# Performance work log

Measured on AMD Instinct MI355X. Metric: run time of the kernel, lower is better.

The kernel has to match this reference:

```python
import jax, jax.numpy as jnp
import numpy as np

N = 50000
E = 800000
IN_DIM = 256
HID = 128
HALF = HID // 2
OUT_DIM = 2


def setup_inputs() -> dict:
    key = jax.random.key(0)
    ks = jax.random.split(key, 16)
    s = lambda fan_in: 1.0 / np.sqrt(fan_in)
    inp = {
        "x": jax.random.normal(ks[0], (N, IN_DIM), dtype=jnp.float32),
        "edge_index": jax.random.randint(ks[1], (2, E), 0, N, dtype=jnp.int64),
        # lin_in: input_dim -> hidden
        "W_in": jax.random.uniform(ks[2], (IN_DIM, HID), jnp.float32, -s(IN_DIM), s(IN_DIM)),
        "b_in": jnp.zeros((HID,), jnp.float32),
        # lin_nor / lin_abnor: half -> hidden
        "W_nor": jax.random.uniform(ks[3], (HALF, HID), jnp.float32, -s(HALF), s(HALF)),
        "b_nor": jnp.zeros((HID,), jnp.float32),
        "W_abnor": jax.random.uniform(ks[4], (HALF, HID), jnp.float32, -s(HALF), s(HALF)),
        "b_abnor": jnp.zeros((HID,), jnp.float32),
        # attention gate
        "W_att": jax.random.uniform(ks[5], (HID, HID), jnp.float32, -s(HID), s(HID)),
        "b_att": jnp.zeros((HID,), jnp.float32),
        "v_att": jax.random.uniform(ks[6], (HID, 1), jnp.float32, -s(HID), s(HID)),
        # update linear
        "W_upd": jax.random.uniform(ks[7], (HID, HID), jnp.float32, -s(HID), s(HID)),
        "b_upd": jnp.zeros((HID,), jnp.float32),
        # classifier
        "W_cls": jax.random.uniform(ks[8], (HID, OUT_DIM), jnp.float32, -s(HID), s(HID)),
        "b_cls": jnp.zeros((OUT_DIM,), jnp.float32),
    }
    return inp


def reference(x, edge_index, W_in, b_in, W_nor, b_nor, W_abnor, b_abnor,
              W_att, b_att, v_att, W_upd, b_upd, W_cls, b_cls):
    n = x.shape[0]
    # add self loops (add_self_loops)
    loops = jnp.tile(jnp.arange(n, dtype=edge_index.dtype), (2, 1))
    ei = jnp.concatenate([edge_index, loops], axis=1)
    row, col = ei[0], ei[1]  # row = source j, col = target i

    # lin_in + leaky_relu (dropout p=0 / eval)
    h = jax.nn.leaky_relu(x @ W_in + b_in)

    # split halves and project
    x_nor = h[:, :HALF] @ W_nor + b_nor      # [N, HID]
    x_abnor = h[:, HALF:] @ W_abnor + b_abnor

    # symmetric normalization by target degree
    deg = jax.ops.segment_sum(jnp.ones_like(col, dtype=h.dtype), col, num_segments=n)
    dinv = jnp.where(deg > 0, jax.lax.rsqrt(jnp.where(deg > 0, deg, 1.0)), 0.0)
    norm = dinv[row] * dinv[col]             # [E']

    # per-edge gather
    xn_j = x_nor[row]                        # [E', HID]
    xa_j = x_abnor[row]

    # denoising attention gate: sigmoid(v^T tanh(W(xn+xa)+b))
    h_att = jnp.tanh((xn_j + xa_j) @ W_att + b_att)
    alpha = jax.nn.sigmoid(h_att @ v_att)    # [E', 1]

    msg = norm[:, None] * (alpha * xn_j + (1.0 - alpha) * xa_j)

    # scatter-add to targets
    aggr = jax.ops.segment_sum(msg, col, num_segments=n)  # [N, HID]

    upd = aggr @ W_upd + b_upd
    out = jax.nn.leaky_relu(upd) @ W_cls + b_cls
    return out
```

## Files before the change

### kernel.cpp

```cpp
#include <hip/hip_runtime.h>

#define N_NODES 50000
#define E_EDGES 800000
#define IN_DIM  256
#define HID     128
#define HALF    64
#define OUT_DIM 2
#define NW      32
#define SLOPE   0.01f

#define ST      132
#define WSLICE  (NW * ST)

#define SCAN_B  512
#define SCAN_NB ((N_NODES + SCAN_B - 1) / SCAN_B)

typedef unsigned int uint32;
typedef __attribute__((ext_vector_type(8)))  __bf16 bf16x8v;
typedef __attribute__((ext_vector_type(16))) float  f32x16;

union BF8 { bf16x8v v; unsigned short s[8]; uint4 q; };

#define FI_F 0
#define FN_F 4096
#define FA_F 5120
#define FT_F 6144
#define FU_F 8192
#define F_TOTAL 10240

__device__ __forceinline__ uint32 rne16u(uint32 u) {
    return (u + 0x7fffu + ((u >> 16) & 1u)) >> 16;
}

__device__ __forceinline__ void split8(const float* f, BF8& hi, BF8& lo) {
    #pragma unroll
    for (int j = 0; j < 8; j++) {
        uint32 uu = __float_as_uint(f[j]);
        uint32 h  = rne16u(uu);
        float  fh = __uint_as_float(h << 16);
        float  r  = f[j] - fh;
        hi.s[j] = (unsigned short)h;
        lo.s[j] = (unsigned short)rne16u(__float_as_uint(r));
    }
}

__device__ __forceinline__ void mfma3(f32x16& acc, bf16x8v ah, bf16x8v al,
                                      bf16x8v bh, bf16x8v bl) {
    acc = __builtin_amdgcn_mfma_f32_32x32x16_bf16(ah, bh, acc, 0, 0, 0);
    acc = __builtin_amdgcn_mfma_f32_32x32x16_bf16(ah, bl, acc, 0, 0, 0);
    acc = __builtin_amdgcn_mfma_f32_32x32x16_bf16(al, bh, acc, 0, 0, 0);
}

__device__ __forceinline__ void mfma_gemm(f32x16* acc, const float* B, int aoff,
                                          int S, int sg0, const uint4* __restrict__ F,
                                          int fbase, int l) {
    const int row = l & 31;
    const int khi = 8 * (l >> 5);
    for (int s = 0; s < S; s++) {
        int k0 = aoff + 16 * s + khi;
        float a8[8];
        *(float4*)&a8[0] = *(const float4*)&B[row * ST + k0];
        *(float4*)&a8[4] = *(const float4*)&B[row * ST + k0 + 4];
        BF8 ah, al; split8(a8, ah, al);
        #pragma unroll
        for (int t = 0; t < 4; t++) {
            int f = fbase + ((sg0 + s) * 4 + t) * 64 + l;
            BF8 bh, bl; bh.q = F[2 * f]; bl.q = F[2 * f + 1];
            mfma3(acc[t], ah.v, al.v, bh.v, bl.v);
        }
    }
}

__device__ __forceinline__ void mfma_gemm2(f32x16* acc, const float* B, int aoff,
                                           int S, int sg0, const uint4* __restrict__ F,
                                           int fbase, int l, int t0) {
    const int row = l & 31;
    const int khi = 8 * (l >> 5);
    for (int s = 0; s < S; s++) {
        int k0 = aoff + 16 * s + khi;
        float a8[8];
        *(float4*)&a8[0] = *(const float4*)&B[row * ST + k0];
        *(float4*)&a8[4] = *(const float4*)&B[row * ST + k0 + 4];
        BF8 ah, al; split8(a8, ah, al);
        #pragma unroll
        for (int tt = 0; tt < 2; tt++) {
            int f = fbase + ((sg0 + s) * 4 + t0 + tt) * 64 + l;
            BF8 bh, bl; bh.q = F[2 * f]; bl.q = F[2 * f + 1];
            mfma3(acc[tt], ah.v, al.v, bh.v, bl.v);
        }
    }
}

__device__ __forceinline__ void initacc(f32x16* acc, const float* __restrict__ b, int col) {
    #pragma unroll
    for (int t = 0; t < 4; t++) {
        float bv = b[32 * t + col];
        #pragma unroll
        for (int r2 = 0; r2 < 16; r2++) acc[t][r2] = bv;
    }
}

__device__ __forceinline__ void initacc2(f32x16* acc, const float* __restrict__ b,
                                         int col, int t0) {
    #pragma unroll
    for (int tt = 0; tt < 2; tt++) {
        float bv = b[32 * (t0 + tt) + col];
        #pragma unroll
        for (int r2 = 0; r2 < 16; r2++) acc[tt][r2] = bv;
    }
}

__device__ __forceinline__ uint32 pack_bf2(float x, float y) {
    return rne16u(__float_as_uint(x)) | (rne16u(__float_as_uint(y)) << 16);
}

__global__ void zero_int_kernel(int* __restrict__ p, int n) {
    int i = blockIdx.x * blockDim.x + threadIdx.x;
    if (i < n) p[i] = 0;
}

__global__ void deg_ticket_kernel(const int* __restrict__ col,
                                  int* __restrict__ cnt, int* __restrict__ ticket) {
    int e = blockIdx.x * blockDim.x + threadIdx.x;
    if (e < E_EDGES) ticket[e] = atomicAdd(&cnt[col[e]], 1);
}

__device__ __forceinline__ int wave_iscan(int v, int l) {
    #pragma unroll
    for (int off = 1; off < 64; off <<= 1) {
        int t = __shfl_up(v, off, 64);
        if (l >= off) v += t;
    }
    return v;
}

__global__ __launch_bounds__(SCAN_B) void scan1_kernel(
    const int* __restrict__ cnt, int* __restrict__ row_start, int* __restrict__ bsum)
{
    __shared__ int wsum[SCAN_B / 64];
    int i = blockIdx.x * SCAN_B + threadIdx.x;
    int v = (i < N_NODES) ? cnt[i] : 0;
    int l = threadIdx.x & 63, w = threadIdx.x >> 6;
    int isc = wave_iscan(v, l);
    if (l == 63) wsum[w] = isc;
    __syncthreads();
    int wo = 0;
    #pragma unroll
    for (int k = 0; k < SCAN_B / 64; k++) wo += (k < w) ? wsum[k] : 0;
    if (i < N_NODES) row_start[i] = wo + isc - v;
    if (threadIdx.x == SCAN_B - 1) bsum[blockIdx.x] = wo + isc;
}

__global__ __launch_bounds__(128) void scan2_kernel(
    int* __restrict__ bsum, int* __restrict__ row_start)
{
    __shared__ int wsum[2];
    int i = threadIdx.x;
    int v = (i < SCAN_NB) ? bsum[i] : 0;
    int l = i & 63, w = i >> 6;
    int isc = wave_iscan(v, l);
    if (l == 63) wsum[w] = isc;
    __syncthreads();
    int wo = (w == 1) ? wsum[0] : 0;
    if (i < SCAN_NB) bsum[i] = wo + isc - v;
    if (i == SCAN_NB - 1) row_start[N_NODES] = wo + isc;
}

__global__ __launch_bounds__(SCAN_B) void scan3_kernel(
    const int* __restrict__ bsum, int* __restrict__ row_start)
{
    int i = blockIdx.x * SCAN_B + threadIdx.x;
    if (i < N_NODES) row_start[i] += bsum[blockIdx.x];
}

__global__ void fill_kernel(const int* __restrict__ ei,
                            const int* __restrict__ row_start,
                            const int* __restrict__ ticket,
                            int* __restrict__ csr_src)
{
    int e = blockIdx.x * blockDim.x + threadIdx.x;
    if (e >= E_EDGES) return;
    int j = ei[e];
    int i = ei[E_EDGES + e];
    csr_src[row_start[i] + ticket[e]] = j;
}

__global__ __launch_bounds__(256) void prep_w_kernel(
    const float* __restrict__ W_in, const float* __restrict__ W_nor,
    const float* __restrict__ W_ab, const float* __restrict__ W_att,
    const float* __restrict__ W_upd,
    uint4* __restrict__ F)
{
    int idx = blockIdx.x * 256 + threadIdx.x;
    const float* W; int fbase, fi;
    if (idx < 4096)       { W = W_in;  fbase = FI_F; fi = idx; }
    else if (idx < 5120)  { W = W_nor; fbase = FN_F; fi = idx - 4096; }
    else if (idx < 6144)  { W = W_ab;  fbase = FA_F; fi = idx - 5120; }
    else if (idx < 8192)  { W = W_att; fbase = FT_F; fi = idx - 6144; }
    else if (idx < 10240) { W = W_upd; fbase = FU_F; fi = idx - 8192; }
    else return;
    int l = fi & 63, st = fi >> 6, t = st & 3, s = st >> 2;
    int k0 = 16 * s + 8 * (l >> 5);
    int c  = 32 * t + (l & 31);
    uint32 hi[8], lo[8];
    #pragma unroll
    for (int j = 0; j < 8; j++) {
        float v = W[(size_t)(k0 + j) * HID + c];
        uint32 uu = __float_as_uint(v);
        uint32 h  = rne16u(uu);
        float  fh = __uint_as_float(h << 16);
        float  r  = v - fh;
        hi[j] = h;
        lo[j] = rne16u(__float_as_uint(r));
    }
    uint4 H, L;
    H.x = hi[0] | (hi[1] << 16); H.y = hi[2] | (hi[3] << 16);
    H.z = hi[4] | (hi[5] << 16); H.w = hi[6] | (hi[7] << 16);
    L.x = lo[0] | (lo[1] << 16); L.y = lo[2] | (lo[3] << 16);
    L.z = lo[4] | (lo[5] << 16); L.w = lo[6] | (lo[7] << 16);
    int f = fbase + fi;
    F[2 * f]     = H;
    F[2 * f + 1] = L;
}

__global__ __launch_bounds__(128, 2) void node_phase_kernel(
    const float* __restrict__ x,
    const float* __restrict__ b_in,  const float* __restrict__ b_nor,
    const float* __restrict__ b_abnor, const float* __restrict__ b_att,
    const float* __restrict__ v_att,
    const int* __restrict__ cnt,
    const uint4* __restrict__ F,
    uint32* __restrict__ u)
{
    __shared__ __align__(16) float B[WSLICE];
    __shared__ float dinvs[NW];
    __shared__ float gpart[2][NW];

    const int tid    = threadIdx.x;
    const int w      = tid >> 6;
    const int l      = tid & 63;
    const int col    = l & 31;
    const int hi     = l >> 5;
    const int t0     = 2 * w;
    const int wnode0 = blockIdx.x * NW;

    if (tid < NW) {
        int nd = wnode0 + tid;
        float c = (nd < N_NODES) ? (float)cnt[nd] : 0.f;
        dinvs[tid] = rsqrtf(c + 1.0f);
    }

    f32x16 hacc[2];
    initacc2(hacc, b_in, col, t0);
    for (int half = 0; half < 2; half++) {
        __syncthreads();
        #pragma unroll
        for (int it = 0; it < 8; it++) {
            int i = it * 128 + tid;
            int rr = i >> 5, kq = i & 31;
            int nd = wnode0 + rr; if (nd >= N_NODES) nd = N_NODES - 1;
            float4 v = *(const float4*)(x + (size_t)nd * IN_DIM + half * 128 + kq * 4);
            *(float4*)&B[rr * ST + kq * 4] = v;
        }
        __syncthreads();
        mfma_gemm2(hacc, B, 0, 8, half * 8, F, FI_F, l, t0);
    }
    __syncthreads();

    #pragma unroll
    for (int tt = 0; tt < 2; tt++) {
        #pragma unroll
        for (int rg = 0; rg < 16; rg++) {
            int rrow = (rg & 3) + 8 * (rg >> 2) + 4 * hi;
            float v = hacc[tt][rg];
            B[rrow * ST + 32 * (t0 + tt) + col] = v > 0.f ? v : SLOPE * v;
        }
    }
    __syncthreads();

    f32x16 xn[2]; initacc2(xn, b_nor, col, t0);
    mfma_gemm2(xn, B, 0, 4, 0, F, FN_F, l, t0);
    f32x16 xa[2]; initacc2(xa, b_abnor, col, t0);
    mfma_gemm2(xa, B, HALF, 4, 0, F, FA_F, l, t0);
    __syncthreads();

    f32x16 d[2];
    #pragma unroll
    for (int tt = 0; tt < 2; tt++) {
        #pragma unroll
        for (int rg = 0; rg < 16; rg++) {
            int rrow = (rg & 3) + 8 * (rg >> 2) + 4 * hi;
            float sv = xn[tt][rg] + xa[tt][rg];
            d[tt][rg] = xn[tt][rg] - xa[tt][rg];
            B[rrow * ST + 32 * (t0 + tt) + col] = sv;
        }
    }
    __syncthreads();

    f32x16 tac[2]; initacc2(tac, b_att, col, t0);
    mfma_gemm2(tac, B, 0, 8, 0, F, FT_F, l, t0);

    float g[16];
    #pragma unroll
    for (int rg = 0; rg < 16; rg++) g[rg] = 0.f;
    #pragma unroll
    for (int tt = 0; tt < 2; tt++) {
        float vv = v_att[32 * (t0 + tt) + col];
        #pragma unroll
        for (int rg = 0; rg < 16; rg++) g[rg] += tanhf(tac[tt][rg]) * vv;
    }
    #pragma unroll
    for (int msk = 16; msk >= 1; msk >>= 1) {
        #pragma unroll
        for (int rg = 0; rg < 16; rg++) g[rg] += __shfl_xor(g[rg], msk, 64);
    }
    if (col == 0) {
        #pragma unroll
        for (int rg = 0; rg < 16; rg++) {
            int rrow = (rg & 3) + 8 * (rg >> 2) + 4 * hi;
            gpart[w][rrow] = g[rg];
        }
    }
    __syncthreads();

    float am[16];
    #pragma unroll
    for (int rg = 0; rg < 16; rg++) {
        int rrow = (rg & 3) + 8 * (rg >> 2) + 4 * hi;
        float gt = gpart[0][rrow] + gpart[1][rrow];
        am[rg] = 1.f / (1.f + expf(-gt)) - 0.5f;
    }

    #pragma unroll
    for (int tt = 0; tt < 2; tt++) {
        #pragma unroll
        for (int rg = 0; rg < 16; rg++) {
            int rrow = (rg & 3) + 8 * (rg >> 2) + 4 * hi;
            int n    = wnode0 + rrow;
            float sv = B[rrow * ST + 32 * (t0 + tt) + col];
            float uv = dinvs[rrow] * (0.5f * sv + am[rg] * d[tt][rg]);
            float pv = __shfl_xor(uv, 1, 64);
            if (((l & 1) == 0) && n < N_NODES) {
                u[(size_t)n * (HID / 2) + 16 * (t0 + tt) + (col >> 1)] = pack_bf2(uv, pv);
            }
        }
    }
}

__global__ __launch_bounds__(256) void gather_kernel(
    const int* __restrict__ row_start, const int* __restrict__ csr_src,
    const uint32* __restrict__ u, float* __restrict__ acc)
{
    int node = blockIdx.x * 4 + (threadIdx.x >> 6);
    int lane = threadIdx.x & 63;
    if (node >= N_NODES) return;

    const size_t RW = HID / 2;
    uint32 v = u[(size_t)node * RW + lane];
    float sx = __uint_as_float(v << 16);
    float sy = __uint_as_float(v & 0xffff0000u);

    int b = row_start[node], e = row_start[node + 1];
    int p = b;
    for (; p + 8 <= e; p += 8) {
        int j0 = csr_src[p + 0], j1 = csr_src[p + 1];
        int j2 = csr_src[p + 2], j3 = csr_src[p + 3];
        int j4 = csr_src[p + 4], j5 = csr_src[p + 5];
        int j6 = csr_src[p + 6], j7 = csr_src[p + 7];
        uint32 v0 = u[(size_t)j0 * RW + lane];
        uint32 v1 = u[(size_t)j1 * RW + lane];
        uint32 v2 = u[(size_t)j2 * RW + lane];
        uint32 v3 = u[(size_t)j3 * RW + lane];
        uint32 v4 = u[(size_t)j4 * RW + lane];
        uint32 v5 = u[(size_t)j5 * RW + lane];
        uint32 v6 = u[(size_t)j6 * RW + lane];
        uint32 v7 = u[(size_t)j7 * RW + lane];
        sx += __uint_as_float(v0 << 16) + __uint_as_float(v1 << 16)
            + __uint_as_float(v2 << 16) + __uint_as_float(v3 << 16)
            + __uint_as_float(v4 << 16) + __uint_as_float(v5 << 16)
            + __uint_as_float(v6 << 16) + __uint_as_float(v7 << 16);
        sy += __uint_as_float(v0 & 0xffff0000u) + __uint_as_float(v1 & 0xffff0000u)
            + __uint_as_float(v2 & 0xffff0000u) + __uint_as_float(v3 & 0xffff0000u)
            + __uint_as_float(v4 & 0xffff0000u) + __uint_as_float(v5 & 0xffff0000u)
            + __uint_as_float(v6 & 0xffff0000u) + __uint_as_float(v7 & 0xffff0000u);
    }
    for (; p < e; p++) {
        int j = csr_src[p];
        uint32 w = u[(size_t)j * RW + lane];
        sx += __uint_as_float(w << 16);
        sy += __uint_as_float(w & 0xffff0000u);
    }
    float2 s = make_float2(sx, sy);
    *(float2*)(acc + (size_t)node * HID + lane * 2) = s;
}

__global__ __launch_bounds__(64, 2) void final_phase_kernel(
    const float* __restrict__ acc, const int* __restrict__ cnt,
    const float* __restrict__ b_upd,
    const float* __restrict__ W_cls, const float* __restrict__ b_cls,
    const uint4* __restrict__ F,
    float* __restrict__ out)
{
    __shared__ __align__(16) float B[WSLICE];

    const int l      = threadIdx.x;
    const int col    = l & 31;
    const int wnode0 = blockIdx.x * NW;

    #pragma unroll
    for (int it = 0; it < 16; it++) {
        int i = it * 64 + l;
        int rr = i >> 5, kq = i & 31;
        int nd = wnode0 + rr; if (nd >= N_NODES) nd = N_NODES - 1;
        float d = rsqrtf((float)cnt[nd] + 1.0f);
        float4 v = *(const float4*)(acc + (size_t)nd * HID + kq * 4);
        v.x *= d; v.y *= d; v.z *= d; v.w *= d;
        *(float4*)&B[rr * ST + kq * 4] = v;
    }

    f32x16 up[4];
    initacc(up, b_upd, col);
    mfma_gemm(up, B, 0, 8, 0, F, FU_F, l);

    #pragma unroll
    for (int t = 0; t < 4; t++) {
        #pragma unroll
        for (int rg = 0; rg < 16; rg++) {
            int rrow = (rg & 3) + 8 * (rg >> 2) + 4 * (l >> 5);
            float v = up[t][rg];
            B[rrow * ST + 32 * t + col] = v > 0.f ? v : SLOPE * v;
        }
    }

    {
        int n = l >> 1, o = l & 1;
        if (wnode0 + n < N_NODES) {
            float s = b_cls[o];
            for (int k = 0; k < HID; k++)
                s = fmaf(B[n * ST + k], W_cls[k * OUT_DIM + o], s);
            out[(size_t)(wnode0 + n) * OUT_DIM + o] = s;
        }
    }
}

extern "C" void kernel_launch(void* const* d_in, const int* in_sizes, int n_in,
                              void* d_out, int out_size, void* d_ws, size_t ws_size,
                              hipStream_t stream)
{
    const float* x       = (const float*)d_in[0];
    const int*   ei      = (const int*)  d_in[1];
    const float* W_in    = (const float*)d_in[2];
    const float* b_in    = (const float*)d_in[3];
    const float* W_nor   = (const float*)d_in[4];
    const float* b_nor   = (const float*)d_in[5];
    const float* W_abnor = (const float*)d_in[6];
    const float* b_abnor = (const float*)d_in[7];
    const float* W_att   = (const float*)d_in[8];
    const float* b_att   = (const float*)d_in[9];
    const float* v_att   = (const float*)d_in[10];
    const float* W_upd   = (const float*)d_in[11];
    const float* b_upd   = (const float*)d_in[12];
    const float* W_cls   = (const float*)d_in[13];
    const float* b_cls   = (const float*)d_in[14];
    float* out = (float*)d_out;

    char* base = (char*)d_ws;
    int*  cnt       = (int*)base;
    int*  row_start = cnt + N_NODES;
    int*  bsum      = row_start + (N_NODES + 1);
    int*  csr_src   = bsum + 128;
    size_t off_u    = (((size_t)(2 * N_NODES + 129 + E_EDGES)) * 4 + 63) & ~(size_t)63;
    uint32* u       = (uint32*)(base + off_u);
    size_t off_acc  = (off_u + (size_t)N_NODES * (HID / 2) * 4 + 63) & ~(size_t)63;
    float* acc      = (float*)(base + off_acc);
    int*   ticket   = (int*)acc;
    size_t off_f    = (off_acc + (size_t)N_NODES * HID * 4 + 63) & ~(size_t)63;
    uint4* F        = (uint4*)(base + off_f);

    const int nblk = (N_NODES + NW - 1) / NW;

    zero_int_kernel<<<(N_NODES + 255) / 256, 256, 0, stream>>>(cnt, N_NODES);
    deg_ticket_kernel<<<(E_EDGES + 255) / 256, 256, 0, stream>>>(ei + E_EDGES, cnt, ticket);
    scan1_kernel<<<SCAN_NB, SCAN_B, 0, stream>>>(cnt, row_start, bsum);
    scan2_kernel<<<1, 128, 0, stream>>>(bsum, row_start);
    scan3_kernel<<<SCAN_NB, SCAN_B, 0, stream>>>(bsum, row_start);
    fill_kernel<<<(E_EDGES + 255) / 256, 256, 0, stream>>>(ei, row_start, ticket, csr_src);
    prep_w_kernel<<<F_TOTAL / 256, 256, 0, stream>>>(W_in, W_nor, W_abnor, W_att, W_upd, F);
    node_phase_kernel<<<nblk, 128, 0, stream>>>(
        x, b_in, b_nor, b_abnor, b_att, v_att, cnt, F, u);
    gather_kernel<<<(N_NODES + 3) / 4, 256, 0, stream>>>(row_start, csr_src, u, acc);
    final_phase_kernel<<<nblk, 64, 0, stream>>>(
        acc, cnt, b_upd, W_cls, b_cls, F, out);
}
```

Baseline: 174.2 us.

## Pre-split activations to bf16 hi/lo in LDS and use four waves per node block

The staged input activations are now split into bf16 hi/lo halves once, when they are written to shared memory, in an MFMA-fragment-friendly layout. Previously every wave re-read the fp32 values and re-split them before each MFMA step. The node-phase kernel moves from 2 waves each owning two 32-column output tiles to 4 waves each owning one tile, with launch bounds raised to 256 threads. This shortens each wave's serial MFMA chain and adds parallelism, at the cost of more barriers and a four-way attention partial reduction. The final phase uses the same pre-split staging for its update GEMM.

New measurement: 170.4 us. -2.2%, faster.

```diff
diff --git a/kernel.cpp b/kernel.cpp
--- a/kernel.cpp
+++ b/kernel.cpp
@@ -51,42 +51,63 @@
     acc = __builtin_amdgcn_mfma_f32_32x32x16_bf16(al, bh, acc, 0, 0, 0);
 }
 
-__device__ __forceinline__ void mfma_gemm(f32x16* acc, const float* B, int aoff,
-                                          int S, int sg0, const uint4* __restrict__ F,
-                                          int fbase, int l) {
-    const int row = l & 31;
-    const int khi = 8 * (l >> 5);
+__device__ __forceinline__ void stage_split4(__bf16* __restrict__ Ahi,
+                                             __bf16* __restrict__ Alo,
+                                             int rr, int k, float4 v) {
+    int s_idx = k >> 4, jb = k & 7, lt = rr + 32 * ((k >> 3) & 1);
+    int base = (s_idx * 64 + lt) * 8 + jb;
+    float f[4] = {v.x, v.y, v.z, v.w};
+    uint32 h[4], lo[4];
+    #pragma unroll
+    for (int j = 0; j < 4; j++) {
+        uint32 uu = __float_as_uint(f[j]);
+        uint32 hh = rne16u(uu);
+        float  fh = __uint_as_float(hh << 16);
+        float  r  = f[j] - fh;
+        h[j] = hh; lo[j] = rne16u(__float_as_uint(r));
+    }
+    *(uint2*)(Ahi + base) = make_uint2(h[0] | (h[1] << 16), h[2] | (h[3] << 16));
+    *(uint2*)(Alo + base) = make_uint2(lo[0] | (lo[1] << 16), lo[2] | (lo[3] << 16));
+}
+
+__device__ __forceinline__ void mfma_gemm1_pre(f32x16& acc,
+        const __bf16* __restrict__ Ahi, const __bf16* __restrict__ Alo,
+        int S, int sg0, const uint4* __restrict__ F, int fbase, int l, int t) {
+    for (int s = 0; s < S; s++) {
+        bf16x8v ah = *(const bf16x8v*)&Ahi[(s * 64 + l) * 8];
+        bf16x8v al = *(const bf16x8v*)&Alo[(s * 64 + l) * 8];
+        int f = fbase + ((sg0 + s) * 4 + t) * 64 + l;
+        BF8 bh, bl; bh.q = F[2 * f]; bl.q = F[2 * f + 1];
+        mfma3(acc, ah, al, bh.v, bl.v);
+    }
+}
+
+__device__ __forceinline__ void mfma_gemm1(f32x16& acc, const float* B, int aoff,
+        int S, int sg0, const uint4* __restrict__ F, int fbase, int l, int t) {
+    const int row = l & 31, khi = 8 * (l >> 5);
     for (int s = 0; s < S; s++) {
         int k0 = aoff + 16 * s + khi;
         float a8[8];
         *(float4*)&a8[0] = *(const float4*)&B[row * ST + k0];
         *(float4*)&a8[4] = *(const float4*)&B[row * ST + k0 + 4];
         BF8 ah, al; split8(a8, ah, al);
+        int f = fbase + ((sg0 + s) * 4 + t) * 64 + l;
+        BF8 bh, bl; bh.q = F[2 * f]; bl.q = F[2 * f + 1];
+        mfma3(acc, ah.v, al.v, bh.v, bl.v);
+    }
+}
+
+__device__ __forceinline__ void mfma_gemm_pre(f32x16* acc,
+        const __bf16* __restrict__ Ahi, const __bf16* __restrict__ Alo,
+        int S, const uint4* __restrict__ F, int fbase, int l) {
+    for (int s = 0; s < S; s++) {
+        bf16x8v ah = *(const bf16x8v*)&Ahi[(s * 64 + l) * 8];
+        bf16x8v al = *(const bf16x8v*)&Alo[(s * 64 + l) * 8];
         #pragma unroll
         for (int t = 0; t < 4; t++) {
-            int f = fbase + ((sg0 + s) * 4 + t) * 64 + l;
+            int f = fbase + (s * 4 + t) * 64 + l;
             BF8 bh, bl; bh.q = F[2 * f]; bl.q = F[2 * f + 1];
-            mfma3(acc[t], ah.v, al.v, bh.v, bl.v);
-        }
-    }
-}
-
-__device__ __forceinline__ void mfma_gemm2(f32x16* acc, const float* B, int aoff,
-                                           int S, int sg0, const uint4* __restrict__ F,
-                                           int fbase, int l, int t0) {
-    const int row = l & 31;
-    const int khi = 8 * (l >> 5);
-    for (int s = 0; s < S; s++) {
-        int k0 = aoff + 16 * s + khi;
-        float a8[8];
-        *(float4*)&a8[0] = *(const float4*)&B[row * ST + k0];
-        *(float4*)&a8[4] = *(const float4*)&B[row * ST + k0 + 4];
-        BF8 ah, al; split8(a8, ah, al);
-        #pragma unroll
-        for (int tt = 0; tt < 2; tt++) {
-            int f = fbase + ((sg0 + s) * 4 + t0 + tt) * 64 + l;
-            BF8 bh, bl; bh.q = F[2 * f]; bl.q = F[2 * f + 1];
-            mfma3(acc[tt], ah.v, al.v, bh.v, bl.v);
+            mfma3(acc[t], ah, al, bh.v, bl.v);
         }
     }
 }
@@ -97,16 +118,6 @@
         float bv = b[32 * t + col];
         #pragma unroll
         for (int r2 = 0; r2 < 16; r2++) acc[t][r2] = bv;
-    }
-}
-
-__device__ __forceinline__ void initacc2(f32x16* acc, const float* __restrict__ b,
-                                         int col, int t0) {
-    #pragma unroll
-    for (int tt = 0; tt < 2; tt++) {
-        float bv = b[32 * (t0 + tt) + col];
-        #pragma unroll
-        for (int r2 = 0; r2 < 16; r2++) acc[tt][r2] = bv;
     }
 }
 
@@ -223,7 +234,7 @@
     F[2 * f + 1] = L;
 }
 
-__global__ __launch_bounds__(128, 2) void node_phase_kernel(
+__global__ __launch_bounds__(256, 4) void node_phase_kernel(
     const float* __restrict__ x,
     const float* __restrict__ b_in,  const float* __restrict__ b_nor,
     const float* __restrict__ b_abnor, const float* __restrict__ b_att,
@@ -232,16 +243,17 @@
     const uint4* __restrict__ F,
     uint32* __restrict__ u)
 {
-    __shared__ __align__(16) float B[WSLICE];
+    __shared__ __align__(16) float smem[WSLICE];
     __shared__ float dinvs[NW];
-    __shared__ float gpart[2][NW];
+    __shared__ float gpart[4][NW];
+    __bf16* Ahi = (__bf16*)smem;
+    __bf16* Alo = (__bf16*)smem + 4096;
 
     const int tid    = threadIdx.x;
     const int w      = tid >> 6;
     const int l      = tid & 63;
     const int col    = l & 31;
     const int hi     = l >> 5;
-    const int t0     = 2 * w;
     const int wnode0 = blockIdx.x * NW;
 
     if (tid < NW) {
@@ -250,64 +262,73 @@
         dinvs[tid] = rsqrtf(c + 1.0f);
     }
 
-    f32x16 hacc[2];
-    initacc2(hacc, b_in, col, t0);
+    f32x16 hacc;
+    {
+        float bv = b_in[32 * w + col];
+        #pragma unroll
+        for (int r2 = 0; r2 < 16; r2++) hacc[r2] = bv;
+    }
     for (int half = 0; half < 2; half++) {
-        __syncthreads();
-        #pragma unroll
-        for (int it = 0; it < 8; it++) {
-            int i = it * 128 + tid;
-            int rr = i >> 5, kq = i & 31;
+        #pragma unroll
+        for (int it = 0; it < 4; it++) {
+            int i = it * 256 + tid;
+            int rr = i >> 5, kq = i & 31, k = 4 * kq;
             int nd = wnode0 + rr; if (nd >= N_NODES) nd = N_NODES - 1;
-            float4 v = *(const float4*)(x + (size_t)nd * IN_DIM + half * 128 + kq * 4);
-            *(float4*)&B[rr * ST + kq * 4] = v;
+            float4 v = *(const float4*)(x + (size_t)nd * IN_DIM + half * 128 + k);
+            stage_split4(Ahi, Alo, rr, k, v);
         }
         __syncthreads();
-        mfma_gemm2(hacc, B, 0, 8, half * 8, F, FI_F, l, t0);
+        mfma_gemm1_pre(hacc, Ahi, Alo, 8, half * 8, F, FI_F, l, w);
+        __syncthreads();
+    }
+
+    float* B = smem;
+    #pragma unroll
+    for (int rg = 0; rg < 16; rg++) {
+        int rrow = (rg & 3) + 8 * (rg >> 2) + 4 * hi;
+        float v = hacc[rg];
+        B[rrow * ST + 32 * w + col] = v > 0.f ? v : SLOPE * v;
     }
     __syncthreads();
 
-    #pragma unroll
-    for (int tt = 0; tt < 2; tt++) {
-        #pragma unroll
-        for (int rg = 0; rg < 16; rg++) {
-            int rrow = (rg & 3) + 8 * (rg >> 2) + 4 * hi;
-            float v = hacc[tt][rg];
-            B[rrow * ST + 32 * (t0 + tt) + col] = v > 0.f ? v : SLOPE * v;
-        }
-    }
+    f32x16 xn, xa;
+    {
+        float bv = b_nor[32 * w + col];
+        #pragma unroll
+        for (int r2 = 0; r2 < 16; r2++) xn[r2] = bv;
+    }
+    mfma_gemm1(xn, B, 0, 4, 0, F, FN_F, l, w);
+    {
+        float bv = b_abnor[32 * w + col];
+        #pragma unroll
+        for (int r2 = 0; r2 < 16; r2++) xa[r2] = bv;
+    }
+    mfma_gemm1(xa, B, HALF, 4, 0, F, FA_F, l, w);
     __syncthreads();
 
-    f32x16 xn[2]; initacc2(xn, b_nor, col, t0);
-    mfma_gemm2(xn, B, 0, 4, 0, F, FN_F, l, t0);
-    f32x16 xa[2]; initacc2(xa, b_abnor, col, t0);
-    mfma_gemm2(xa, B, HALF, 4, 0, F, FA_F, l, t0);
+    f32x16 d;
+    #pragma unroll
+    for (int rg = 0; rg < 16; rg++) {
+        int rrow = (rg & 3) + 8 * (rg >> 2) + 4 * hi;
+        float sv = xn[rg] + xa[rg];
+        d[rg] = xn[rg] - xa[rg];
+        B[rrow * ST + 32 * w + col] = sv;
+    }
     __syncthreads();
 
-    f32x16 d[2];
-    #pragma unroll
-    for (int tt = 0; tt < 2; tt++) {
-        #pragma unroll
-        for (int rg = 0; rg < 16; rg++) {
-            int rrow = (rg & 3) + 8 * (rg >> 2) + 4 * hi;
-            float sv = xn[tt][rg] + xa[tt][rg];
-            d[tt][rg] = xn[tt][rg] - xa[tt][rg];
-            B[rrow * ST + 32 * (t0 + tt) + col] = sv;
-        }
-    }
-    __syncthreads();
-
-    f32x16 tac[2]; initacc2(tac, b_att, col, t0);
-    mfma_gemm2(tac, B, 0, 8, 0, F, FT_F, l, t0);
+    f32x16 tac;
+    {
+        float bv = b_att[32 * w + col];
+        #pragma unroll
+        for (int r2 = 0; r2 < 16; r2++) tac[r2] = bv;
+    }
+    mfma_gemm1(tac, B, 0, 8, 0, F, FT_F, l, w);
 
     float g[16];
-    #pragma unroll
-    for (int rg = 0; rg < 16; rg++) g[rg] = 0.f;
-    #pragma unroll
-    for (int tt = 0; tt < 2; tt++) {
-        float vv = v_att[32 * (t0 + tt) + col];
-        #pragma unroll
-        for (int rg = 0; rg < 16; rg++) g[rg] += tanhf(tac[tt][rg]) * vv;
+    {
+        float vv = v_att[32 * w + col];
+        #pragma unroll
+        for (int rg = 0; rg < 16; rg++) g[rg] = tanhf(tac[rg]) * vv;
     }
     #pragma unroll
     for (int msk = 16; msk >= 1; msk >>= 1) {
@@ -327,22 +348,19 @@
     #pragma unroll
     for (int rg = 0; rg < 16; rg++) {
         int rrow = (rg & 3) + 8 * (rg >> 2) + 4 * hi;
-        float gt = gpart[0][rrow] + gpart[1][rrow];
+        float gt = gpart[0][rrow] + gpart[1][rrow] + gpart[2][rrow] + gpart[3][rrow];
         am[rg] = 1.f / (1.f + expf(-gt)) - 0.5f;
     }
 
     #pragma unroll
-    for (int tt = 0; tt < 2; tt++) {
-        #pragma unroll
-        for (int rg = 0; rg < 16; rg++) {
-            int rrow = (rg & 3) + 8 * (rg >> 2) + 4 * hi;
-            int n    = wnode0 + rrow;
-            float sv = B[rrow * ST + 32 * (t0 + tt) + col];
-            float uv = dinvs[rrow] * (0.5f * sv + am[rg] * d[tt][rg]);
-            float pv = __shfl_xor(uv, 1, 64);
-            if (((l & 1) == 0) && n < N_NODES) {
-                u[(size_t)n * (HID / 2) + 16 * (t0 + tt) + (col >> 1)] = pack_bf2(uv, pv);
-            }
+    for (int rg = 0; rg < 16; rg++) {
+        int rrow = (rg & 3) + 8 * (rg >> 2) + 4 * hi;
+        int n    = wnode0 + rrow;
+        float sv = B[rrow * ST + 32 * w + col];
+        float uv = dinvs[rrow] * (0.5f * sv + am[rg] * d[rg]);
+        float pv = __shfl_xor(uv, 1, 64);
+        if (((l & 1) == 0) && n < N_NODES) {
+            u[(size_t)n * (HID / 2) + 16 * w + (col >> 1)] = pack_bf2(uv, pv);
         }
     }
 }
@@ -401,7 +419,9 @@
     const uint4* __restrict__ F,
     float* __restrict__ out)
 {
-    __shared__ __align__(16) float B[WSLICE];
+    __shared__ __align__(16) float smem[WSLICE];
+    __bf16* Ahi = (__bf16*)smem;
+    __bf16* Alo = (__bf16*)smem + 4096;
 
     const int l      = threadIdx.x;
     const int col    = l & 31;
@@ -410,18 +430,19 @@
     #pragma unroll
     for (int it = 0; it < 16; it++) {
         int i = it * 64 + l;
-        int rr = i >> 5, kq = i & 31;
+        int rr = i >> 5, kq = i & 31, k = 4 * kq;
         int nd = wnode0 + rr; if (nd >= N_NODES) nd = N_NODES - 1;
-        float d = rsqrtf((float)cnt[nd] + 1.0f);
-        float4 v = *(const float4*)(acc + (size_t)nd * HID + kq * 4);
-        v.x *= d; v.y *= d; v.z *= d; v.w *= d;
-        *(float4*)&B[rr * ST + kq * 4] = v;
+        float dv = rsqrtf((float)cnt[nd] + 1.0f);
+        float4 v = *(const float4*)(acc + (size_t)nd * HID + k);
+        v.x *= dv; v.y *= dv; v.z *= dv; v.w *= dv;
+        stage_split4(Ahi, Alo, rr, k, v);
     }
 
     f32x16 up[4];
     initacc(up, b_upd, col);
-    mfma_gemm(up, B, 0, 8, 0, F, FU_F, l);
-
+    mfma_gemm_pre(up, Ahi, Alo, 8, F, FU_F, l);
+
+    float* B = smem;
     #pragma unroll
     for (int t = 0; t < 4; t++) {
         #pragma unroll
@@ -486,7 +507,7 @@
     scan3_kernel<<<SCAN_NB, SCAN_B, 0, stream>>>(bsum, row_start);
     fill_kernel<<<(E_EDGES + 255) / 256, 256, 0, stream>>>(ei, row_start, ticket, csr_src);
     prep_w_kernel<<<F_TOTAL / 256, 256, 0, stream>>>(W_in, W_nor, W_abnor, W_att, W_upd, F);
-    node_phase_kernel<<<nblk, 128, 0, stream>>>(
+    node_phase_kernel<<<nblk, 256, 0, stream>>>(
         x, b_in, b_nor, b_abnor, b_att, v_att, cnt, F, u);
     gather_kernel<<<(N_NODES + 3) / 4, 256, 0, stream>>>(row_start, csr_src, u, acc);
     final_phase_kernel<<<nblk, 64, 0, stream>>>(
```
